# Kernel tuning notes

Hardware: AMD Instinct MI355X
Metric: run time of the kernel (lower is better)

Reference implementation:

```python
import jax, jax.numpy as jnp
import numpy as np

N_NODES = 50000
N_EDGES = 800000
NFEAT, NHID, NCLASS = 512, 128, 40


def _glorot(key, fan_in, fan_out):
    # mimics the usual GCN uniform init: U(-1/sqrt(fan_out), 1/sqrt(fan_out))
    stdv = 1.0 / np.sqrt(fan_out)
    return jax.random.uniform(key, (fan_in, fan_out), jnp.float32, -stdv, stdv)


def setup_inputs() -> dict:
    key = jax.random.key(0)
    ks = jax.random.split(key, 8)
    x = jax.random.normal(ks[0], (N_NODES, NFEAT), jnp.float32)
    edge_src = jax.random.randint(ks[1], (N_EDGES,), 0, N_NODES)
    edge_dst = jax.random.randint(ks[2], (N_EDGES,), 0, N_NODES)
    edge_weight = jax.random.uniform(ks[3], (N_EDGES,), jnp.float32)
    W1 = _glorot(ks[4], NFEAT, NHID)
    b1 = jnp.zeros((NHID,), jnp.float32)
    W2 = _glorot(ks[5], NHID, NCLASS)
    b2 = jnp.zeros((NCLASS,), jnp.float32)
    return {"x": x, "edge_src": edge_src, "edge_dst": edge_dst,
            "edge_weight": edge_weight, "W1": W1, "b1": b1, "W2": W2, "b2": b2}


def _gcn_layer(x, W, b, edge_src, edge_dst, edge_weight):
    # support = x @ W ; out = spmm(adj, support) + b
    support = x @ W                                   # [N, F_out]
    msgs = support[edge_src] * edge_weight[:, None]   # [E, F_out]
    agg = jax.ops.segment_sum(msgs, edge_dst, num_segments=N_NODES)
    return agg + b


def reference(x, edge_src, edge_dst, edge_weight, W1, b1, W2, b2):
    h = _gcn_layer(x, W1, b1, edge_src, edge_dst, edge_weight)
    h = jax.nn.relu(h)
    # F.dropout(training=False) -> identity in eval mode
    out = _gcn_layer(h, W2, b2, edge_src, edge_dst, edge_weight)
    return out
```

## Files before the change

### kernel.cpp

```cpp
#include <hip/hip_runtime.h>


#define F0 512
#define F1 128
#define F2 40
#define F2P 48

typedef short bf16x8 __attribute__((ext_vector_type(8)));
typedef float f32x4 __attribute__((ext_vector_type(4)));

static __device__ __forceinline__ unsigned short f2b(float f){
    union { float f; unsigned int u; } x; x.f = f;
    unsigned int u = x.u;
    unsigned int r = (u + 0x7fffu + ((u >> 16) & 1u)) >> 16;
    return (unsigned short)r;
}
static __device__ __forceinline__ unsigned short f2b_fast(float f){
    return (unsigned short)((__float_as_uint(f) + 0x8000u) >> 16);
}
static __device__ __forceinline__ unsigned int pack2(float a, float b){
    unsigned int ua = __float_as_uint(a) + 0x8000u;
    unsigned int ub = __float_as_uint(b) + 0x8000u;
    return __builtin_amdgcn_perm(ub, ua, 0x07060302u);
}
static __device__ __forceinline__ bf16x8 pack8(float4 v0, float4 v1){
    union { bf16x8 v; unsigned int d[4]; } r;
    r.d[0] = pack2(v0.x, v0.y);
    r.d[1] = pack2(v0.z, v0.w);
    r.d[2] = pack2(v1.x, v1.y);
    r.d[3] = pack2(v1.z, v1.w);
    return r.v;
}
static __device__ __forceinline__ float b2f(unsigned short h){
    union { unsigned int u; float f; } x; x.u = ((unsigned int)h) << 16; return x.f;
}
static __device__ __forceinline__ unsigned short f2h(float f){
    union { _Float16 h; unsigned short u; } x; x.h = (_Float16)f; return x.u;
}
static __device__ __forceinline__ float h2f(unsigned short u){
    union { unsigned short u; _Float16 h; } x; x.u = u; return (float)x.h;
}

__global__ void prep_w(const float* __restrict__ W1, const float* __restrict__ W2,
                       unsigned short* __restrict__ W1t, unsigned short* __restrict__ W2t,
                       int* __restrict__ cnt8, int n8, int* __restrict__ gflag){
    int idx = blockIdx.x*256 + threadIdx.x;
    if (idx < n8) cnt8[idx] = 0;
    if (idx < 64) gflag[idx] = 0;
    if (idx < F0*F1){
        int k = idx >> 7, n = idx & 127;
        W1t[(size_t)n*F0 + k] = f2b(W1[idx]);
    } else if (idx < F0*F1 + F2P*F1){
        int j = idx - F0*F1;
        int n = j >> 7, k = j & 127;
        float v = (n < F2) ? W2[(size_t)k*F2 + n] : 0.f;
        W2t[j] = f2b(v);
    }
}

__global__ void xconv(const float* __restrict__ X, unsigned short* __restrict__ Xb, int n8){
    int stride = gridDim.x*256;
    for (int i = blockIdx.x*256 + threadIdx.x; i < n8; i += stride){
        const float4* p = (const float4*)(X + (size_t)i*8);
        float4 v0 = p[0], v1 = p[1];
        *(bf16x8*)&Xb[(size_t)i*8] = pack8(v0, v1);
    }
}

__global__ void hist_kernel(const int* __restrict__ dst, int* __restrict__ cnt8,
                            unsigned short* __restrict__ slot, int E){
    int e = blockIdx.x*256 + threadIdx.x;
    if (e < E){
        int d = dst[e];
        slot[e] = (unsigned short)atomicAdd(&cnt8[d*8 + (e & 7)], 1);
    }
}

__global__ __launch_bounds__(256) void gemm1_mfma(const unsigned short* __restrict__ Xb,
                                                  const unsigned short* __restrict__ W1t,
                                                  unsigned short* __restrict__ S1, int M){
    __shared__ unsigned short sB[128*136];
    int tid = threadIdx.x;
    int wave = tid >> 6, lane = tid & 63;
    int quad = lane >> 4, l16 = lane & 15;
    int row0 = blockIdx.x * 64;
    int arow = min(row0 + wave*16 + l16, M-1);
    const unsigned short* xrow = Xb + (size_t)arow * F0;

    f32x4 acc[8];
    #pragma unroll
    for (int c=0;c<8;c++) acc[c] = (f32x4){0.f,0.f,0.f,0.f};

    #pragma unroll 1
    for (int p = 0; p < 4; p++){
        __syncthreads();
        bf16x8 a0 = *(const bf16x8*)(xrow + p*128 + 0*32 + quad*8);
        bf16x8 a1 = *(const bf16x8*)(xrow + p*128 + 1*32 + quad*8);
        bf16x8 a2 = *(const bf16x8*)(xrow + p*128 + 2*32 + quad*8);
        bf16x8 a3 = *(const bf16x8*)(xrow + p*128 + 3*32 + quad*8);
        #pragma unroll
        for (int i=0;i<8;i++){
            int idx = tid + i*256;
            int nn = idx >> 4, c8 = idx & 15;
            *(float4*)&sB[nn*136 + c8*8] =
                *(const float4*)&W1t[(size_t)nn*F0 + p*128 + c8*8];
        }
        __syncthreads();
        #pragma unroll
        for (int c=0;c<8;c++){
            bf16x8 b0 = *(bf16x8*)&sB[(c*16 + l16)*136 + 0*32 + quad*8];
            acc[c] = __builtin_amdgcn_mfma_f32_16x16x32_bf16(a0, b0, acc[c], 0, 0, 0);
            bf16x8 b1 = *(bf16x8*)&sB[(c*16 + l16)*136 + 1*32 + quad*8];
            acc[c] = __builtin_amdgcn_mfma_f32_16x16x32_bf16(a1, b1, acc[c], 0, 0, 0);
            bf16x8 b2 = *(bf16x8*)&sB[(c*16 + l16)*136 + 2*32 + quad*8];
            acc[c] = __builtin_amdgcn_mfma_f32_16x16x32_bf16(a2, b2, acc[c], 0, 0, 0);
            bf16x8 b3 = *(bf16x8*)&sB[(c*16 + l16)*136 + 3*32 + quad*8];
            acc[c] = __builtin_amdgcn_mfma_f32_16x16x32_bf16(a3, b3, acc[c], 0, 0, 0);
        }
    }
    #pragma unroll
    for (int c=0;c<8;c++){
        #pragma unroll
        for (int r=0;r<4;r++){
            int grow = row0 + wave*16 + quad*4 + r;
            if (grow < M) S1[(size_t)grow*F1 + c*16 + l16] = f2b_fast(acc[c][r]);
        }
    }
}

__global__ void scan_fused(const int* __restrict__ cnt8, int* __restrict__ offs,
                           int* __restrict__ sbase, int* __restrict__ gflag,
                           int n, int E){
    __shared__ int sd[256];
    __shared__ int s_excl;
    int tid = threadIdx.x, bid = blockIdx.x;
    int base = bid*1024 + tid*4;

    int t[4];
    int lpr[4][8];
    #pragma unroll
    for (int j=0;j<4;j++){
        int node = base+j;
        int tot = 0;
        #pragma unroll
        for (int k=0;k<8;k++) lpr[j][k] = 0;
        if (node < n){
            int4 c0 = *(const int4*)&cnt8[(size_t)node*8];
            int4 c1 = *(const int4*)&cnt8[(size_t)node*8+4];
            int run;
            lpr[j][0] = 0;   run  = c0.x;
            lpr[j][1] = run; run += c0.y;
            lpr[j][2] = run; run += c0.z;
            lpr[j][3] = run; run += c0.w;
            lpr[j][4] = run; run += c1.x;
            lpr[j][5] = run; run += c1.y;
            lpr[j][6] = run; run += c1.z;
            lpr[j][7] = run; run += c1.w;
            tot = run;
        }
        t[j] = tot;
    }
    int v1 = t[0], v2 = t[0]+t[1], v3 = v2+t[2];
    int s = v3 + t[3];
    sd[tid] = s; __syncthreads();
    for (int off=1; off<256; off<<=1){
        int tt = (tid>=off) ? sd[tid-off] : 0;
        __syncthreads();
        sd[tid] += tt;
        __syncthreads();
    }
    int excl = sd[tid] - s;
    int btot = sd[255];

    if (tid == 0)
        __hip_atomic_store(&gflag[bid], btot + 1, __ATOMIC_RELEASE, __HIP_MEMORY_SCOPE_AGENT);
    if (tid < 64){
        int v = 0;
        if (tid < bid){
            int g;
            do {
                g = __hip_atomic_load(&gflag[tid], __ATOMIC_ACQUIRE, __HIP_MEMORY_SCOPE_AGENT);
                if (g == 0) __builtin_amdgcn_s_sleep(1);
            } while (g == 0);
            v = g - 1;
        }
        #pragma unroll
        for (int o=1; o<64; o<<=1) v += __shfl_xor(v, o);
        if (tid == 0) s_excl = v;
    }
    __syncthreads();

    int node_off[4] = {0, v1, v2, v3};
    int gexcl = s_excl + excl;
    #pragma unroll
    for (int j=0;j<4;j++){
        int node = base+j;
        if (node < n){
            int o = gexcl + node_off[j];
            offs[node] = o;
            int4 s0, s1;
            s0.x = o + lpr[j][0]; s0.y = o + lpr[j][1];
            s0.z = o + lpr[j][2]; s0.w = o + lpr[j][3];
            s1.x = o + lpr[j][4]; s1.y = o + lpr[j][5];
            s1.z = o + lpr[j][6]; s1.w = o + lpr[j][7];
            *(int4*)&sbase[(size_t)node*8]   = s0;
            *(int4*)&sbase[(size_t)node*8+4] = s1;
        }
    }
    if (bid == 0 && tid == 0) offs[n] = E;
}

__global__ void scatter_kernel(const int* __restrict__ src, const int* __restrict__ dst,
                               const float* __restrict__ w,
                               const int* __restrict__ sbase,
                               const unsigned short* __restrict__ slot,
                               unsigned int* __restrict__ edges, int E){
    int e = blockIdx.x*256+threadIdx.x;
    if (e<E){
        int d = dst[e];
        int pos = sbase[d*8 + (e & 7)] + (int)slot[e];
        edges[pos] = ((unsigned int)src[e] << 16) | (unsigned int)f2h(w[e]);
    }
}

__global__ void agg1_kernel(const unsigned short* __restrict__ S1, const int* __restrict__ offs,
                            const unsigned int* __restrict__ edges,
                            const float* __restrict__ b1, unsigned short* __restrict__ H, int n){
    int node = blockIdx.x*4 + (threadIdx.x >> 6);
    int lane = threadIdx.x & 63;
    if (node >= n) return;
    int half = lane >> 5, fl = lane & 31;
    int e0 = offs[node], e1 = offs[node+1];
    double a0=0.0, a1=0.0, a2=0.0, a3=0.0;
    int e = e0;
    for (; e+8 <= e1; e += 8){
        unsigned int rA = edges[e   + half];
        unsigned int rB = edges[e+2 + half];
        unsigned int rC = edges[e+4 + half];
        unsigned int rD = edges[e+6 + half];
        ushort4 vA = *(const ushort4*)&S1[((size_t)(rA>>16))*F1 + fl*4];
        ushort4 vB = *(const ushort4*)&S1[((size_t)(rB>>16))*F1 + fl*4];
        ushort4 vC = *(const ushort4*)&S1[((size_t)(rC>>16))*F1 + fl*4];
        ushort4 vD = *(const ushort4*)&S1[((size_t)(rD>>16))*F1 + fl*4];
        double wA = h2f((unsigned short)rA), wB = h2f((unsigned short)rB);
        double wC = h2f((unsigned short)rC), wD = h2f((unsigned short)rD);
        a0 += wA*b2f(vA.x) + wB*b2f(vB.x) + wC*b2f(vC.x) + wD*b2f(vD.x);
        a1 += wA*b2f(vA.y) + wB*b2f(vB.y) + wC*b2f(vC.y) + wD*b2f(vD.y);
        a2 += wA*b2f(vA.z) + wB*b2f(vB.z) + wC*b2f(vC.z) + wD*b2f(vD.z);
        a3 += wA*b2f(vA.w) + wB*b2f(vB.w) + wC*b2f(vC.w) + wD*b2f(vD.w);
    }
    for (; e < e1; e += 2){
        int ee = e + half;
        if (ee < e1){
            unsigned int r = edges[ee];
            ushort4 v = *(const ushort4*)&S1[((size_t)(r>>16))*F1 + fl*4];
            double w = h2f((unsigned short)r);
            a0 += w*b2f(v.x); a1 += w*b2f(v.y); a2 += w*b2f(v.z); a3 += w*b2f(v.w);
        }
    }
    a0 += __shfl_down(a0, 32);
    a1 += __shfl_down(a1, 32);
    a2 += __shfl_down(a2, 32);
    a3 += __shfl_down(a3, 32);
    if (lane < 32){
        float4 bb = *(const float4*)&b1[fl*4];
        float o0 = (float)(a0 + (double)bb.x);
        float o1 = (float)(a1 + (double)bb.y);
        float o2 = (float)(a2 + (double)bb.z);
        float o3 = (float)(a3 + (double)bb.w);
        o0 = o0>0.f?o0:0.f; o1 = o1>0.f?o1:0.f;
        o2 = o2>0.f?o2:0.f; o3 = o3>0.f?o3:0.f;
        union { ushort4 v; unsigned int d[2]; } o;
        o.d[0] = pack2(o0, o1);
        o.d[1] = pack2(o2, o3);
        *(ushort4*)&H[(size_t)node*F1 + fl*4] = o.v;
    }
}

__global__ __launch_bounds__(256) void gemm2_mfma(const unsigned short* __restrict__ H,
                                                  const unsigned short* __restrict__ W2t,
                                                  unsigned short* __restrict__ S2, int M){
    __shared__ unsigned short sB[48][136];
    int tid = threadIdx.x;
    int wave = tid >> 6, lane = tid & 63;
    int quad = lane >> 4, l16 = lane & 15;
    for (int i = tid; i < 48*16; i += 256){
        int nn = i >> 4, p = i & 15;
        *(float4*)&sB[nn][p*8] = *(const float4*)&W2t[(size_t)nn*F1 + p*8];
    }
    int row0 = blockIdx.x * 64;
    int myrow = row0 + wave*16 + l16;
    int arow = min(myrow, M-1);
    const unsigned short* hrow = H + (size_t)arow * F1;
    bf16x8 a[4];
    #pragma unroll
    for (int ks=0; ks<4; ks++) a[ks] = *(const bf16x8*)(hrow + ks*32 + quad*8);
    __syncthreads();
    f32x4 acc[3];
    #pragma unroll
    for (int c=0;c<3;c++) acc[c] = (f32x4){0.f,0.f,0.f,0.f};
    #pragma unroll
    for (int ks=0; ks<4; ks++){
        #pragma unroll
        for (int c=0;c<3;c++){
            bf16x8 b = *(bf16x8*)&sB[c*16 + l16][ks*32 + quad*8];
            acc[c] = __builtin_amdgcn_mfma_f32_16x16x32_bf16(a[ks], b, acc[c], 0, 0, 0);
        }
    }
    #pragma unroll
    for (int c=0;c<3;c++){
        #pragma unroll
        for (int r=0;r<4;r++){
            int grow = row0 + wave*16 + quad*4 + r;
            if (grow < M) S2[(size_t)grow*F2P + c*16 + l16] = f2b_fast(acc[c][r]);
        }
    }
}

__global__ void agg2_kernel(const unsigned short* __restrict__ S2, const int* __restrict__ offs,
                            const unsigned int* __restrict__ edges,
                            const float* __restrict__ b2, float* __restrict__ out, int n){
    int node = blockIdx.x*4 + (threadIdx.x >> 6);
    int lane = threadIdx.x & 63;
    if (node >= n) return;
    int grp = lane >> 4, gl = lane & 15;
    bool act = gl < 10;
    int e0 = offs[node], e1 = offs[node+1];
    double a0=0.0, a1=0.0, a2=0.0, a3=0.0;
    for (int e = e0; e < e1; e += 4){
        int ee = e + grp;
        if (ee < e1 && act){
            unsigned int r = edges[ee];
            ushort4 v = *(const ushort4*)&S2[((size_t)(r>>16))*F2P + gl*4];
            double w = h2f((unsigned short)r);
            a0 += w*b2f(v.x); a1 += w*b2f(v.y); a2 += w*b2f(v.z); a3 += w*b2f(v.w);
        }
    }
    a0 += __shfl_down(a0, 32); a0 += __shfl_down(a0, 16);
    a1 += __shfl_down(a1, 32); a1 += __shfl_down(a1, 16);
    a2 += __shfl_down(a2, 32); a2 += __shfl_down(a2, 16);
    a3 += __shfl_down(a3, 32); a3 += __shfl_down(a3, 16);
    if (lane < 10){
        float4 bb = *(const float4*)&b2[lane*4];
        float4 o;
        o.x = (float)(a0 + (double)bb.x);
        o.y = (float)(a1 + (double)bb.y);
        o.z = (float)(a2 + (double)bb.z);
        o.w = (float)(a3 + (double)bb.w);
        *(float4*)&out[(size_t)node*F2 + lane*4] = o;
    }
}

extern "C" void kernel_launch(void* const* d_in, const int* in_sizes, int n_in,
                              void* d_out, int out_size, void* d_ws, size_t ws_size,
                              hipStream_t stream){
    const float* x    = (const float*)d_in[0];
    const int*   esrc = (const int*)d_in[1];
    const int*   edst = (const int*)d_in[2];
    const float* ew   = (const float*)d_in[3];
    const float* W1   = (const float*)d_in[4];
    const float* b1   = (const float*)d_in[5];
    const float* W2   = (const float*)d_in[6];
    const float* b2   = (const float*)d_in[7];
    float* out = (float*)d_out;
    int N = in_sizes[0] / F0;
    int E = in_sizes[1];

    char* ws = (char*)d_ws;
    size_t off = 0;
    auto alloc = [&](size_t bytes)->void*{
        void* p = ws + off; off += (bytes + 255) & ~(size_t)255; return p;
    };
    unsigned short* Xb = (unsigned short*)alloc(sizeof(unsigned short)*(size_t)N*F0);
    unsigned short* S1 = (unsigned short*)alloc(sizeof(unsigned short)*(size_t)N*F1);
    unsigned short* H  = (unsigned short*)alloc(sizeof(unsigned short)*(size_t)N*F1);
    unsigned short* S2 = (unsigned short*)alloc(sizeof(unsigned short)*(size_t)N*F2P);
    unsigned short* W1t = (unsigned short*)alloc(sizeof(unsigned short)*F1*F0);
    unsigned short* W2t = (unsigned short*)alloc(sizeof(unsigned short)*F2P*F1);
    int*   offs  = (int*)alloc(sizeof(int)*(size_t)(N+1));
    int*   cnt8  = (int*)alloc(sizeof(int)*(size_t)N*8);
    int*   sbase = (int*)alloc(sizeof(int)*(size_t)N*8);
    unsigned short* slot = (unsigned short*)alloc(sizeof(unsigned short)*(size_t)E);
    unsigned int* edges = (unsigned int*)alloc(sizeof(unsigned int)*(size_t)E);
    int*   gflag = (int*)alloc(sizeof(int)*64);

    int n8 = N*8;
    int prep_items = n8 > (F0*F1 + F2P*F1) ? n8 : (F0*F1 + F2P*F1);
    prep_w<<<(prep_items+255)/256,256,0,stream>>>(W1, W2, W1t, W2t, cnt8, n8, gflag);

    hist_kernel<<<(E+255)/256,256,0,stream>>>(edst, cnt8, slot, E);

    xconv<<<2048,256,0,stream>>>(x, Xb, N*F0/8);

    int gemm_nb = (N+63)/64;
    gemm1_mfma<<<gemm_nb,256,0,stream>>>(Xb, W1t, S1, N);

    int nb = (N+1023)/1024;
    scan_fused<<<nb,256,0,stream>>>(cnt8, offs, sbase, gflag, N, E);
    scatter_kernel<<<(E+255)/256,256,0,stream>>>(esrc, edst, ew, sbase, slot, edges, E);

    agg1_kernel<<<(N+3)/4,256,0,stream>>>(S1, offs, edges, b1, H, N);
    gemm2_mfma<<<gemm_nb,256,0,stream>>>(H, W2t, S2, N);
    agg2_kernel<<<(N+3)/4,256,0,stream>>>(S2, offs, edges, b2, out, N);
}
```

Baseline: 337.0 us.

## Fuse all GCN stages into one persistent kernel with grid barriers

Replaces the chain of nine kernel launches with a single persistent kernel of 1024 blocks that moves between phases using a software grid barrier. The fp32→bf16 conversion of X is folded into the GEMM1 A-operand load, which removes the Xb intermediate buffer and one full pass over X. The histogram is placed in the same phase as GEMM1. This removes launch gaps and an extra memory round trip, at the cost of grid-barrier overhead, lower per-phase parallelism, and the assumption that all 1024 blocks are co-resident. The spin waits are capped, so if a block is not resident a phase can go ahead early and produce wrong results instead of hanging.

```diff
diff --git a/kernel.cpp b/kernel.cpp
--- a/kernel.cpp
+++ b/kernel.cpp
@@ -5,6 +5,9 @@
 #define F1 128
 #define F2 40
 #define F2P 48
+#define GRID 1024
+#define GSZ (GRID*256)
+#define SPIN_CAP 200000
 
 typedef short bf16x8 __attribute__((ext_vector_type(8)));
 typedef float f32x4 __attribute__((ext_vector_type(4)));
@@ -41,313 +44,325 @@
     union { unsigned short u; _Float16 h; } x; x.u = u; return (float)x.h;
 }
 
-__global__ void prep_w(const float* __restrict__ W1, const float* __restrict__ W2,
-                       unsigned short* __restrict__ W1t, unsigned short* __restrict__ W2t,
-                       int* __restrict__ cnt8, int n8, int* __restrict__ gflag){
-    int idx = blockIdx.x*256 + threadIdx.x;
-    if (idx < n8) cnt8[idx] = 0;
-    if (idx < 64) gflag[idx] = 0;
-    if (idx < F0*F1){
-        int k = idx >> 7, n = idx & 127;
-        W1t[(size_t)n*F0 + k] = f2b(W1[idx]);
-    } else if (idx < F0*F1 + F2P*F1){
-        int j = idx - F0*F1;
-        int n = j >> 7, k = j & 127;
-        float v = (n < F2) ? W2[(size_t)k*F2 + n] : 0.f;
-        W2t[j] = f2b(v);
-    }
-}
-
-__global__ void xconv(const float* __restrict__ X, unsigned short* __restrict__ Xb, int n8){
-    int stride = gridDim.x*256;
-    for (int i = blockIdx.x*256 + threadIdx.x; i < n8; i += stride){
-        const float4* p = (const float4*)(X + (size_t)i*8);
-        float4 v0 = p[0], v1 = p[1];
-        *(bf16x8*)&Xb[(size_t)i*8] = pack8(v0, v1);
-    }
-}
-
-__global__ void hist_kernel(const int* __restrict__ dst, int* __restrict__ cnt8,
-                            unsigned short* __restrict__ slot, int E){
-    int e = blockIdx.x*256 + threadIdx.x;
-    if (e < E){
-        int d = dst[e];
-        slot[e] = (unsigned short)atomicAdd(&cnt8[d*8 + (e & 7)], 1);
-    }
-}
-
-__global__ __launch_bounds__(256) void gemm1_mfma(const unsigned short* __restrict__ Xb,
-                                                  const unsigned short* __restrict__ W1t,
-                                                  unsigned short* __restrict__ S1, int M){
+static __device__ __forceinline__ void gbar(int* __restrict__ bar){
+    __syncthreads();
+    if (threadIdx.x == 0){
+        int g = __hip_atomic_load(&bar[1], __ATOMIC_RELAXED, __HIP_MEMORY_SCOPE_AGENT);
+        int old = __hip_atomic_fetch_add(&bar[0], 1, __ATOMIC_ACQ_REL, __HIP_MEMORY_SCOPE_AGENT);
+        if (old == GRID-1){
+            __hip_atomic_store(&bar[0], 0, __ATOMIC_RELAXED, __HIP_MEMORY_SCOPE_AGENT);
+            __hip_atomic_store(&bar[1], g+1, __ATOMIC_RELEASE, __HIP_MEMORY_SCOPE_AGENT);
+        } else {
+            int cur, tries = 0;
+            do {
+                __builtin_amdgcn_s_sleep(2);
+                cur = __hip_atomic_load(&bar[1], __ATOMIC_ACQUIRE, __HIP_MEMORY_SCOPE_AGENT);
+            } while (cur == g && ++tries < SPIN_CAP);
+        }
+    }
+    __syncthreads();
+}
+
+__global__ void init_bar(int* __restrict__ bar, int* __restrict__ gflag){
+    int t = threadIdx.x;
+    if (t < 2)  bar[t] = 0;
+    if (t < 64) gflag[t] = 0;
+}
+
+__global__ __launch_bounds__(256, 4) void mega(
+    const float* __restrict__ X,
+    const float* __restrict__ W1, const float* __restrict__ W2,
+    const float* __restrict__ b1, const float* __restrict__ b2,
+    const int* __restrict__ esrc, const int* __restrict__ edst,
+    const float* __restrict__ ew,
+    unsigned short* __restrict__ W1t, unsigned short* __restrict__ W2t,
+    unsigned short* __restrict__ S1, unsigned short* __restrict__ H,
+    unsigned short* __restrict__ S2,
+    int* __restrict__ offs, int* __restrict__ cnt8, int* __restrict__ sbase,
+    unsigned short* __restrict__ slot, unsigned int* __restrict__ edges,
+    int* __restrict__ gflag, int* __restrict__ bar, float* __restrict__ out,
+    int N, int E, int gemm_nt, int nb)
+{
     __shared__ unsigned short sB[128*136];
-    int tid = threadIdx.x;
+    __shared__ int sd[256];
+    __shared__ int s_excl;
+
+    int tid = threadIdx.x, bid = blockIdx.x;
+    int gid = bid*256 + tid;
     int wave = tid >> 6, lane = tid & 63;
     int quad = lane >> 4, l16 = lane & 15;
-    int row0 = blockIdx.x * 64;
-    int arow = min(row0 + wave*16 + l16, M-1);
-    const unsigned short* xrow = Xb + (size_t)arow * F0;
-
-    f32x4 acc[8];
-    #pragma unroll
-    for (int c=0;c<8;c++) acc[c] = (f32x4){0.f,0.f,0.f,0.f};
-
-    #pragma unroll 1
-    for (int p = 0; p < 4; p++){
-        __syncthreads();
-        bf16x8 a0 = *(const bf16x8*)(xrow + p*128 + 0*32 + quad*8);
-        bf16x8 a1 = *(const bf16x8*)(xrow + p*128 + 1*32 + quad*8);
-        bf16x8 a2 = *(const bf16x8*)(xrow + p*128 + 2*32 + quad*8);
-        bf16x8 a3 = *(const bf16x8*)(xrow + p*128 + 3*32 + quad*8);
+
+    {
+        int n8_4 = N*2;
+        for (int i = gid; i < n8_4; i += GSZ) ((int4*)cnt8)[i] = (int4){0,0,0,0};
+        for (int i = gid; i < F0*F1; i += GSZ){
+            int k = i >> 7, n = i & 127;
+            W1t[n*F0 + k] = f2b(W1[i]);
+        }
+        if (gid < F2P*F1){
+            int n = gid >> 7, k = gid & 127;
+            float v = (n < F2) ? W2[(size_t)k*F2 + n] : 0.f;
+            W2t[gid] = f2b(v);
+        }
+    }
+    gbar(bar);
+
+    for (int t = bid; t < gemm_nt; t += GRID){
+        int row0 = t * 64;
+        int arow = min(row0 + wave*16 + l16, N-1);
+        const float* xrow = X + (size_t)arow * F0;
+        f32x4 acc[8];
         #pragma unroll
-        for (int i=0;i<8;i++){
-            int idx = tid + i*256;
-            int nn = idx >> 4, c8 = idx & 15;
-            *(float4*)&sB[nn*136 + c8*8] =
-                *(const float4*)&W1t[(size_t)nn*F0 + p*128 + c8*8];
-        }
-        __syncthreads();
+        for (int c=0;c<8;c++) acc[c] = (f32x4){0.f,0.f,0.f,0.f};
+
+        #pragma unroll 1
+        for (int p = 0; p < 4; p++){
+            __syncthreads();
+            const float* xr = xrow + p*128 + quad*8;
+            float4 v0 = *(const float4*)(xr +  0), v1 = *(const float4*)(xr +  4);
+            float4 v2 = *(const float4*)(xr + 32), v3 = *(const float4*)(xr + 36);
+            float4 v4 = *(const float4*)(xr + 64), v5 = *(const float4*)(xr + 68);
+            float4 v6 = *(const float4*)(xr + 96), v7 = *(const float4*)(xr + 100);
+            #pragma unroll
+            for (int i=0;i<8;i++){
+                int idx = tid + i*256;
+                int nn = idx >> 4, c8 = idx & 15;
+                *(float4*)&sB[nn*136 + c8*8] =
+                    *(const float4*)&W1t[(size_t)nn*F0 + p*128 + c8*8];
+            }
+            __syncthreads();
+            bf16x8 a0 = pack8(v0, v1), a1 = pack8(v2, v3);
+            bf16x8 a2 = pack8(v4, v5), a3 = pack8(v6, v7);
+            #pragma unroll
+            for (int c=0;c<8;c++){
+                bf16x8 b0 = *(bf16x8*)&sB[(c*16 + l16)*136 + 0*32 + quad*8];
+                acc[c] = __builtin_amdgcn_mfma_f32_16x16x32_bf16(a0, b0, acc[c], 0, 0, 0);
+                bf16x8 b1 = *(bf16x8*)&sB[(c*16 + l16)*136 + 1*32 + quad*8];
+                acc[c] = __builtin_amdgcn_mfma_f32_16x16x32_bf16(a1, b1, acc[c], 0, 0, 0);
+                bf16x8 b2 = *(bf16x8*)&sB[(c*16 + l16)*136 + 2*32 + quad*8];
+                acc[c] = __builtin_amdgcn_mfma_f32_16x16x32_bf16(a2, b2, acc[c], 0, 0, 0);
+                bf16x8 b3 = *(bf16x8*)&sB[(c*16 + l16)*136 + 3*32 + quad*8];
+                acc[c] = __builtin_amdgcn_mfma_f32_16x16x32_bf16(a3, b3, acc[c], 0, 0, 0);
+            }
+        }
         #pragma unroll
         for (int c=0;c<8;c++){
-            bf16x8 b0 = *(bf16x8*)&sB[(c*16 + l16)*136 + 0*32 + quad*8];
-            acc[c] = __builtin_amdgcn_mfma_f32_16x16x32_bf16(a0, b0, acc[c], 0, 0, 0);
-            bf16x8 b1 = *(bf16x8*)&sB[(c*16 + l16)*136 + 1*32 + quad*8];
-            acc[c] = __builtin_amdgcn_mfma_f32_16x16x32_bf16(a1, b1, acc[c], 0, 0, 0);
-            bf16x8 b2 = *(bf16x8*)&sB[(c*16 + l16)*136 + 2*32 + quad*8];
-            acc[c] = __builtin_amdgcn_mfma_f32_16x16x32_bf16(a2, b2, acc[c], 0, 0, 0);
-            bf16x8 b3 = *(bf16x8*)&sB[(c*16 + l16)*136 + 3*32 + quad*8];
-            acc[c] = __builtin_amdgcn_mfma_f32_16x16x32_bf16(a3, b3, acc[c], 0, 0, 0);
-        }
-    }
-    #pragma unroll
-    for (int c=0;c<8;c++){
+            #pragma unroll
+            for (int r=0;r<4;r++){
+                int grow = row0 + wave*16 + quad*4 + r;
+                if (grow < N) S1[(size_t)grow*F1 + c*16 + l16] = f2b_fast(acc[c][r]);
+            }
+        }
+    }
+    for (int e = gid; e < E; e += GSZ){
+        int d = edst[e];
+        slot[e] = (unsigned short)atomicAdd(&cnt8[d*8 + (e & 7)], 1);
+    }
+    gbar(bar);
+
+    if (bid < nb){
+        int base = bid*1024 + tid*4;
+        int t4[4];
+        int lpr[4][8];
         #pragma unroll
-        for (int r=0;r<4;r++){
-            int grow = row0 + wave*16 + quad*4 + r;
-            if (grow < M) S1[(size_t)grow*F1 + c*16 + l16] = f2b_fast(acc[c][r]);
-        }
-    }
-}
-
-__global__ void scan_fused(const int* __restrict__ cnt8, int* __restrict__ offs,
-                           int* __restrict__ sbase, int* __restrict__ gflag,
-                           int n, int E){
-    __shared__ int sd[256];
-    __shared__ int s_excl;
-    int tid = threadIdx.x, bid = blockIdx.x;
-    int base = bid*1024 + tid*4;
-
-    int t[4];
-    int lpr[4][8];
-    #pragma unroll
-    for (int j=0;j<4;j++){
-        int node = base+j;
-        int tot = 0;
+        for (int j=0;j<4;j++){
+            int node = base+j;
+            int tot = 0;
+            #pragma unroll
+            for (int k=0;k<8;k++) lpr[j][k] = 0;
+            if (node < N){
+                int4 c0 = *(const int4*)&cnt8[(size_t)node*8];
+                int4 c1 = *(const int4*)&cnt8[(size_t)node*8+4];
+                int run;
+                lpr[j][0] = 0;   run  = c0.x;
+                lpr[j][1] = run; run += c0.y;
+                lpr[j][2] = run; run += c0.z;
+                lpr[j][3] = run; run += c0.w;
+                lpr[j][4] = run; run += c1.x;
+                lpr[j][5] = run; run += c1.y;
+                lpr[j][6] = run; run += c1.z;
+                lpr[j][7] = run; run += c1.w;
+                tot = run;
+            }
+            t4[j] = tot;
+        }
+        int v1 = t4[0], v2 = t4[0]+t4[1], v3 = v2+t4[2];
+        int s = v3 + t4[3];
+        sd[tid] = s; __syncthreads();
+        for (int off=1; off<256; off<<=1){
+            int tt = (tid>=off) ? sd[tid-off] : 0;
+            __syncthreads();
+            sd[tid] += tt;
+            __syncthreads();
+        }
+        int excl = sd[tid] - s;
+        int btot = sd[255];
+
+        if (tid == 0)
+            __hip_atomic_store(&gflag[bid], btot + 1, __ATOMIC_RELEASE, __HIP_MEMORY_SCOPE_AGENT);
+        if (tid < 64){
+            int v = 0;
+            if (tid < bid){
+                int g, tries = 0;
+                do {
+                    g = __hip_atomic_load(&gflag[tid], __ATOMIC_ACQUIRE, __HIP_MEMORY_SCOPE_AGENT);
+                    if (g == 0) __builtin_amdgcn_s_sleep(1);
+                } while (g == 0 && ++tries < SPIN_CAP);
+                v = g - 1;
+            }
+            #pragma unroll
+            for (int o=1; o<64; o<<=1) v += __shfl_xor(v, o);
+            if (tid == 0) s_excl = v;
+        }
+        __syncthreads();
+
+        int node_off[4] = {0, v1, v2, v3};
+        int gexcl = s_excl + excl;
         #pragma unroll
-        for (int k=0;k<8;k++) lpr[j][k] = 0;
-        if (node < n){
-            int4 c0 = *(const int4*)&cnt8[(size_t)node*8];
-            int4 c1 = *(const int4*)&cnt8[(size_t)node*8+4];
-            int run;
-            lpr[j][0] = 0;   run  = c0.x;
-            lpr[j][1] = run; run += c0.y;
-            lpr[j][2] = run; run += c0.z;
-            lpr[j][3] = run; run += c0.w;
-            lpr[j][4] = run; run += c1.x;
-            lpr[j][5] = run; run += c1.y;
-            lpr[j][6] = run; run += c1.z;
-            lpr[j][7] = run; run += c1.w;
-            tot = run;
-        }
-        t[j] = tot;
-    }
-    int v1 = t[0], v2 = t[0]+t[1], v3 = v2+t[2];
-    int s = v3 + t[3];
-    sd[tid] = s; __syncthreads();
-    for (int off=1; off<256; off<<=1){
-        int tt = (tid>=off) ? sd[tid-off] : 0;
+        for (int j=0;j<4;j++){
+            int node = base+j;
+            if (node < N){
+                int o = gexcl + node_off[j];
+                offs[node] = o;
+                int4 s0, s1;
+                s0.x = o + lpr[j][0]; s0.y = o + lpr[j][1];
+                s0.z = o + lpr[j][2]; s0.w = o + lpr[j][3];
+                s1.x = o + lpr[j][4]; s1.y = o + lpr[j][5];
+                s1.z = o + lpr[j][6]; s1.w = o + lpr[j][7];
+                *(int4*)&sbase[(size_t)node*8]   = s0;
+                *(int4*)&sbase[(size_t)node*8+4] = s1;
+            }
+        }
+        if (bid == 0 && tid == 0) offs[N] = E;
+    }
+    gbar(bar);
+
+    for (int e = gid; e < E; e += GSZ){
+        int d = edst[e];
+        int pos = sbase[d*8 + (e & 7)] + (int)slot[e];
+        pos = min(max(pos, 0), E-1);
+        edges[pos] = ((unsigned int)esrc[e] << 16) | (unsigned int)f2h(ew[e]);
+    }
+    gbar(bar);
+
+    {
+        int half = lane >> 5, fl = lane & 31;
+        for (int node = bid*4 + wave; node < N; node += GRID*4){
+            int e0 = offs[node], e1 = offs[node+1];
+            double a0=0.0, a1=0.0, a2=0.0, a3=0.0;
+            int e = e0;
+            for (; e+8 <= e1; e += 8){
+                unsigned int rA = edges[e   + half];
+                unsigned int rB = edges[e+2 + half];
+                unsigned int rC = edges[e+4 + half];
+                unsigned int rD = edges[e+6 + half];
+                ushort4 vA = *(const ushort4*)&S1[((size_t)(rA>>16))*F1 + fl*4];
+                ushort4 vB = *(const ushort4*)&S1[((size_t)(rB>>16))*F1 + fl*4];
+                ushort4 vC = *(const ushort4*)&S1[((size_t)(rC>>16))*F1 + fl*4];
+                ushort4 vD = *(const ushort4*)&S1[((size_t)(rD>>16))*F1 + fl*4];
+                double wA = h2f((unsigned short)rA), wB = h2f((unsigned short)rB);
+                double wC = h2f((unsigned short)rC), wD = h2f((unsigned short)rD);
+                a0 += wA*b2f(vA.x) + wB*b2f(vB.x) + wC*b2f(vC.x) + wD*b2f(vD.x);
+                a1 += wA*b2f(vA.y) + wB*b2f(vB.y) + wC*b2f(vC.y) + wD*b2f(vD.y);
+                a2 += wA*b2f(vA.z) + wB*b2f(vB.z) + wC*b2f(vC.z) + wD*b2f(vD.z);
+                a3 += wA*b2f(vA.w) + wB*b2f(vB.w) + wC*b2f(vC.w) + wD*b2f(vD.w);
+            }
+            for (; e < e1; e += 2){
+                int ee = e + half;
+                if (ee < e1){
+                    unsigned int r = edges[ee];
+                    ushort4 v = *(const ushort4*)&S1[((size_t)(r>>16))*F1 + fl*4];
+                    double w = h2f((unsigned short)r);
+                    a0 += w*b2f(v.x); a1 += w*b2f(v.y); a2 += w*b2f(v.z); a3 += w*b2f(v.w);
+                }
+            }
+            a0 += __shfl_down(a0, 32);
+            a1 += __shfl_down(a1, 32);
+            a2 += __shfl_down(a2, 32);
+            a3 += __shfl_down(a3, 32);
+            if (lane < 32){
+                float4 bb = *(const float4*)&b1[fl*4];
+                float o0 = (float)(a0 + (double)bb.x);
+                float o1 = (float)(a1 + (double)bb.y);
+                float o2 = (float)(a2 + (double)bb.z);
+                float o3 = (float)(a3 + (double)bb.w);
+                o0 = o0>0.f?o0:0.f; o1 = o1>0.f?o1:0.f;
+                o2 = o2>0.f?o2:0.f; o3 = o3>0.f?o3:0.f;
+                union { ushort4 v; unsigned int d[2]; } o;
+                o.d[0] = pack2(o0, o1);
+                o.d[1] = pack2(o2, o3);
+                *(ushort4*)&H[(size_t)node*F1 + fl*4] = o.v;
+            }
+        }
+    }
+    gbar(bar);
+
+    {
+        unsigned short (*sB2)[136] = (unsigned short(*)[136])sB;
+        for (int i = tid; i < 48*16; i += 256){
+            int nn = i >> 4, p = i & 15;
+            *(float4*)&sB2[nn][p*8] = *(const float4*)&W2t[(size_t)nn*F1 + p*8];
+        }
         __syncthreads();
-        sd[tid] += tt;
-        __syncthreads();
-    }
-    int excl = sd[tid] - s;
-    int btot = sd[255];
-
-    if (tid == 0)
-        __hip_atomic_store(&gflag[bid], btot + 1, __ATOMIC_RELEASE, __HIP_MEMORY_SCOPE_AGENT);
-    if (tid < 64){
-        int v = 0;
-        if (tid < bid){
-            int g;
-            do {
-                g = __hip_atomic_load(&gflag[tid], __ATOMIC_ACQUIRE, __HIP_MEMORY_SCOPE_AGENT);
-                if (g == 0) __builtin_amdgcn_s_sleep(1);
-            } while (g == 0);
-            v = g - 1;
-        }
-        #pragma unroll
-        for (int o=1; o<64; o<<=1) v += __shfl_xor(v, o);
-        if (tid == 0) s_excl = v;
-    }
-    __syncthreads();
-
-    int node_off[4] = {0, v1, v2, v3};
-    int gexcl = s_excl + excl;
-    #pragma unroll
-    for (int j=0;j<4;j++){
-        int node = base+j;
-        if (node < n){
-            int o = gexcl + node_off[j];
-            offs[node] = o;
-            int4 s0, s1;
-            s0.x = o + lpr[j][0]; s0.y = o + lpr[j][1];
-            s0.z = o + lpr[j][2]; s0.w = o + lpr[j][3];
-            s1.x = o + lpr[j][4]; s1.y = o + lpr[j][5];
-            s1.z = o + lpr[j][6]; s1.w = o + lpr[j][7];
-            *(int4*)&sbase[(size_t)node*8]   = s0;
-            *(int4*)&sbase[(size_t)node*8+4] = s1;
-        }
-    }
-    if (bid == 0 && tid == 0) offs[n] = E;
-}
-
-__global__ void scatter_kernel(const int* __restrict__ src, const int* __restrict__ dst,
-                               const float* __restrict__ w,
-                               const int* __restrict__ sbase,
-                               const unsigned short* __restrict__ slot,
-                               unsigned int* __restrict__ edges, int E){
-    int e = blockIdx.x*256+threadIdx.x;
-    if (e<E){
-        int d = dst[e];
-        int pos = sbase[d*8 + (e & 7)] + (int)slot[e];
-        edges[pos] = ((unsigned int)src[e] << 16) | (unsigned int)f2h(w[e]);
-    }
-}
-
-__global__ void agg1_kernel(const unsigned short* __restrict__ S1, const int* __restrict__ offs,
-                            const unsigned int* __restrict__ edges,
-                            const float* __restrict__ b1, unsigned short* __restrict__ H, int n){
-    int node = blockIdx.x*4 + (threadIdx.x >> 6);
-    int lane = threadIdx.x & 63;
-    if (node >= n) return;
-    int half = lane >> 5, fl = lane & 31;
-    int e0 = offs[node], e1 = offs[node+1];
-    double a0=0.0, a1=0.0, a2=0.0, a3=0.0;
-    int e = e0;
-    for (; e+8 <= e1; e += 8){
-        unsigned int rA = edges[e   + half];
-        unsigned int rB = edges[e+2 + half];
-        unsigned int rC = edges[e+4 + half];
-        unsigned int rD = edges[e+6 + half];
-        ushort4 vA = *(const ushort4*)&S1[((size_t)(rA>>16))*F1 + fl*4];
-        ushort4 vB = *(const ushort4*)&S1[((size_t)(rB>>16))*F1 + fl*4];
-        ushort4 vC = *(const ushort4*)&S1[((size_t)(rC>>16))*F1 + fl*4];
-        ushort4 vD = *(const ushort4*)&S1[((size_t)(rD>>16))*F1 + fl*4];
-        double wA = h2f((unsigned short)rA), wB = h2f((unsigned short)rB);
-        double wC = h2f((unsigned short)rC), wD = h2f((unsigned short)rD);
-        a0 += wA*b2f(vA.x) + wB*b2f(vB.x) + wC*b2f(vC.x) + wD*b2f(vD.x);
-        a1 += wA*b2f(vA.y) + wB*b2f(vB.y) + wC*b2f(vC.y) + wD*b2f(vD.y);
-        a2 += wA*b2f(vA.z) + wB*b2f(vB.z) + wC*b2f(vC.z) + wD*b2f(vD.z);
-        a3 += wA*b2f(vA.w) + wB*b2f(vB.w) + wC*b2f(vC.w) + wD*b2f(vD.w);
-    }
-    for (; e < e1; e += 2){
-        int ee = e + half;
-        if (ee < e1){
-            unsigned int r = edges[ee];
-            ushort4 v = *(const ushort4*)&S1[((size_t)(r>>16))*F1 + fl*4];
-            double w = h2f((unsigned short)r);
-            a0 += w*b2f(v.x); a1 += w*b2f(v.y); a2 += w*b2f(v.z); a3 += w*b2f(v.w);
-        }
-    }
-    a0 += __shfl_down(a0, 32);
-    a1 += __shfl_down(a1, 32);
-    a2 += __shfl_down(a2, 32);
-    a3 += __shfl_down(a3, 32);
-    if (lane < 32){
-        float4 bb = *(const float4*)&b1[fl*4];
-        float o0 = (float)(a0 + (double)bb.x);
-        float o1 = (float)(a1 + (double)bb.y);
-        float o2 = (float)(a2 + (double)bb.z);
-        float o3 = (float)(a3 + (double)bb.w);
-        o0 = o0>0.f?o0:0.f; o1 = o1>0.f?o1:0.f;
-        o2 = o2>0.f?o2:0.f; o3 = o3>0.f?o3:0.f;
-        union { ushort4 v; unsigned int d[2]; } o;
-        o.d[0] = pack2(o0, o1);
-        o.d[1] = pack2(o2, o3);
-        *(ushort4*)&H[(size_t)node*F1 + fl*4] = o.v;
-    }
-}
-
-__global__ __launch_bounds__(256) void gemm2_mfma(const unsigned short* __restrict__ H,
-                                                  const unsigned short* __restrict__ W2t,
-                                                  unsigned short* __restrict__ S2, int M){
-    __shared__ unsigned short sB[48][136];
-    int tid = threadIdx.x;
-    int wave = tid >> 6, lane = tid & 63;
-    int quad = lane >> 4, l16 = lane & 15;
-    for (int i = tid; i < 48*16; i += 256){
-        int nn = i >> 4, p = i & 15;
-        *(float4*)&sB[nn][p*8] = *(const float4*)&W2t[(size_t)nn*F1 + p*8];
-    }
-    int row0 = blockIdx.x * 64;
-    int myrow = row0 + wave*16 + l16;
-    int arow = min(myrow, M-1);
-    const unsigned short* hrow = H + (size_t)arow * F1;
-    bf16x8 a[4];
-    #pragma unroll
-    for (int ks=0; ks<4; ks++) a[ks] = *(const bf16x8*)(hrow + ks*32 + quad*8);
-    __syncthreads();
-    f32x4 acc[3];
-    #pragma unroll
-    for (int c=0;c<3;c++) acc[c] = (f32x4){0.f,0.f,0.f,0.f};
-    #pragma unroll
-    for (int ks=0; ks<4; ks++){
-        #pragma unroll
-        for (int c=0;c<3;c++){
-            bf16x8 b = *(bf16x8*)&sB[c*16 + l16][ks*32 + quad*8];
-            acc[c] = __builtin_amdgcn_mfma_f32_16x16x32_bf16(a[ks], b, acc[c], 0, 0, 0);
-        }
-    }
-    #pragma unroll
-    for (int c=0;c<3;c++){
-        #pragma unroll
-        for (int r=0;r<4;r++){
-            int grow = row0 + wave*16 + quad*4 + r;
-            if (grow < M) S2[(size_t)grow*F2P + c*16 + l16] = f2b_fast(acc[c][r]);
-        }
-    }
-}
-
-__global__ void agg2_kernel(const unsigned short* __restrict__ S2, const int* __restrict__ offs,
-                            const unsigned int* __restrict__ edges,
-                            const float* __restrict__ b2, float* __restrict__ out, int n){
-    int node = blockIdx.x*4 + (threadIdx.x >> 6);
-    int lane = threadIdx.x & 63;
-    if (node >= n) return;
-    int grp = lane >> 4, gl = lane & 15;
-    bool act = gl < 10;
-    int e0 = offs[node], e1 = offs[node+1];
-    double a0=0.0, a1=0.0, a2=0.0, a3=0.0;
-    for (int e = e0; e < e1; e += 4){
-        int ee = e + grp;
-        if (ee < e1 && act){
-            unsigned int r = edges[ee];
-            ushort4 v = *(const ushort4*)&S2[((size_t)(r>>16))*F2P + gl*4];
-            double w = h2f((unsigned short)r);
-            a0 += w*b2f(v.x); a1 += w*b2f(v.y); a2 += w*b2f(v.z); a3 += w*b2f(v.w);
-        }
-    }
-    a0 += __shfl_down(a0, 32); a0 += __shfl_down(a0, 16);
-    a1 += __shfl_down(a1, 32); a1 += __shfl_down(a1, 16);
-    a2 += __shfl_down(a2, 32); a2 += __shfl_down(a2, 16);
-    a3 += __shfl_down(a3, 32); a3 += __shfl_down(a3, 16);
-    if (lane < 10){
-        float4 bb = *(const float4*)&b2[lane*4];
-        float4 o;
-        o.x = (float)(a0 + (double)bb.x);
-        o.y = (float)(a1 + (double)bb.y);
-        o.z = (float)(a2 + (double)bb.z);
-        o.w = (float)(a3 + (double)bb.w);
-        *(float4*)&out[(size_t)node*F2 + lane*4] = o;
+        for (int t = bid; t < gemm_nt; t += GRID){
+            int row0 = t * 64;
+            int arow = min(row0 + wave*16 + l16, N-1);
+            const unsigned short* hrow = H + (size_t)arow * F1;
+            bf16x8 a[4];
+            #pragma unroll
+            for (int ks=0; ks<4; ks++) a[ks] = *(const bf16x8*)(hrow + ks*32 + quad*8);
+            f32x4 acc[3];
+            #pragma unroll
+            for (int c=0;c<3;c++) acc[c] = (f32x4){0.f,0.f,0.f,0.f};
+            #pragma unroll
+            for (int ks=0; ks<4; ks++){
+                #pragma unroll
+                for (int c=0;c<3;c++){
+                    bf16x8 b = *(bf16x8*)&sB2[c*16 + l16][ks*32 + quad*8];
+                    acc[c] = __builtin_amdgcn_mfma_f32_16x16x32_bf16(a[ks], b, acc[c], 0, 0, 0);
+                }
+            }
+            #pragma unroll
+            for (int c=0;c<3;c++){
+                #pragma unroll
+                for (int r=0;r<4;r++){
+                    int grow = row0 + wave*16 + quad*4 + r;
+                    if (grow < N) S2[(size_t)grow*F2P + c*16 + l16] = f2b_fast(acc[c][r]);
+                }
+            }
+        }
+    }
+    gbar(bar);
+
+    {
+        int grp = lane >> 4, gl = lane & 15;
+        bool act = gl < 10;
+        for (int node = bid*4 + wave; node < N; node += GRID*4){
+            int e0 = offs[node], e1 = offs[node+1];
+            double a0=0.0, a1=0.0, a2=0.0, a3=0.0;
+            for (int e = e0; e < e1; e += 4){
+                int ee = e + grp;
+                if (ee < e1 && act){
+                    unsigned int r = edges[ee];
+                    ushort4 v = *(const ushort4*)&S2[((size_t)(r>>16))*F2P + gl*4];
+                    double w = h2f((unsigned short)r);
+                    a0 += w*b2f(v.x); a1 += w*b2f(v.y); a2 += w*b2f(v.z); a3 += w*b2f(v.w);
+                }
+            }
+            a0 += __shfl_down(a0, 32); a0 += __shfl_down(a0, 16);
+            a1 += __shfl_down(a1, 32); a1 += __shfl_down(a1, 16);
+            a2 += __shfl_down(a2, 32); a2 += __shfl_down(a2, 16);
+            a3 += __shfl_down(a3, 32); a3 += __shfl_down(a3, 16);
+            if (lane < 10){
+                float4 bb = *(const float4*)&b2[lane*4];
+                float4 o;
+                o.x = (float)(a0 + (double)bb.x);
+                o.y = (float)(a1 + (double)bb.y);
+                o.z = (float)(a2 + (double)bb.z);
+                o.w = (float)(a3 + (double)bb.w);
+                *(float4*)&out[(size_t)node*F2 + lane*4] = o;
+            }
+        }
     }
 }
 
@@ -371,7 +386,6 @@
     auto alloc = [&](size_t bytes)->void*{
         void* p = ws + off; off += (bytes + 255) & ~(size_t)255; return p;
     };
-    unsigned short* Xb = (unsigned short*)alloc(sizeof(unsigned short)*(size_t)N*F0);
     unsigned short* S1 = (unsigned short*)alloc(sizeof(unsigned short)*(size_t)N*F1);
     unsigned short* H  = (unsigned short*)alloc(sizeof(unsigned short)*(size_t)N*F1);
     unsigned short* S2 = (unsigned short*)alloc(sizeof(unsigned short)*(size_t)N*F2P);
@@ -383,23 +397,14 @@
     unsigned short* slot = (unsigned short*)alloc(sizeof(unsigned short)*(size_t)E);
     unsigned int* edges = (unsigned int*)alloc(sizeof(unsigned int)*(size_t)E);
     int*   gflag = (int*)alloc(sizeof(int)*64);
-
-    int n8 = N*8;
-    int prep_items = n8 > (F0*F1 + F2P*F1) ? n8 : (F0*F1 + F2P*F1);
-    prep_w<<<(prep_items+255)/256,256,0,stream>>>(W1, W2, W1t, W2t, cnt8, n8, gflag);
-
-    hist_kernel<<<(E+255)/256,256,0,stream>>>(edst, cnt8, slot, E);
-
-    xconv<<<2048,256,0,stream>>>(x, Xb, N*F0/8);
-
-    int gemm_nb = (N+63)/64;
-    gemm1_mfma<<<gemm_nb,256,0,stream>>>(Xb, W1t, S1, N);
-
+    int*   bar   = (int*)alloc(sizeof(int)*64);
+
+    int gemm_nt = (N+63)/64;
     int nb = (N+1023)/1024;
-    scan_fused<<<nb,256,0,stream>>>(cnt8, offs, sbase, gflag, N, E);
-    scatter_kernel<<<(E+255)/256,256,0,stream>>>(esrc, edst, ew, sbase, slot, edges, E);
-
-    agg1_kernel<<<(N+3)/4,256,0,stream>>>(S1, offs, edges, b1, H, N);
-    gemm2_mfma<<<gemm_nb,256,0,stream>>>(H, W2t, S2, N);
-    agg2_kernel<<<(N+3)/4,256,0,stream>>>(S2, offs, edges, b2, out, N);
-}
+
+    init_bar<<<1,64,0,stream>>>(bar, gflag);
+    mega<<<GRID,256,0,stream>>>(x, W1, W2, b1, b2, esrc, edst, ew,
+                                W1t, W2t, S1, H, S2,
+                                offs, cnt8, sbase, slot, edges,
+                                gflag, bar, out, N, E, gemm_nt, nb);
+}
```

After: 1.295 ms. +284.3%, slower.
